# Kernel optimization log

Hardware: AMD Instinct MI355X
Metric: run time of the kernel (lower is better)

## Reference

```python
import jax, jax.numpy as jnp
import numpy as np

DIM = 128
H = 8
NEG_SLOPE = 0.2
SCALE = 12.0
N_ITEMS = 81920
E_INT = 163840
N_T = 4096
NUM_NODE = 40000


def _normalize(x, eps=1e-12):
    n = jnp.linalg.norm(x, axis=-1, keepdims=True)
    return x / jnp.maximum(n, eps)


def _gat(feat, src, dst, fc_w, attn_l, attn_r, bias):
    # GATConv with residual (Identity, since in_feats == out_feats) and bias.
    N = feat.shape[0]
    fs = (feat @ fc_w.T).reshape(N, H, DIM)                # [N,H,D]
    el = jnp.einsum('nhd,hd->nh', fs, attn_l)              # [N,H]
    er = jnp.einsum('nhd,hd->nh', fs, attn_r)              # [N,H]
    e = el[src] + er[dst]                                  # u_add_v -> [E,H]
    e = jnp.where(e >= 0, e, NEG_SLOPE * e)                # leaky_relu
    # edge_softmax grouped by destination node
    emax = jax.ops.segment_max(e, dst, num_segments=N)
    ex = jnp.exp(e - emax[dst])
    denom = jax.ops.segment_sum(ex, dst, num_segments=N)
    a = ex / denom[dst]                                    # [E,H]
    # u_mul_e + sum aggregation
    m = fs[src] * a[:, :, None]                            # [E,H,D]
    rst = jax.ops.segment_sum(m, dst, num_segments=N)      # [N,H,D]
    rst = rst + feat[:, None, :] + bias.reshape(1, H, DIM)
    return rst


def setup_inputs() -> dict:
    key = jax.random.key(0)
    ks = jax.random.split(key, 20)
    stdv = 1.0 / np.sqrt(DIM)

    def unif(k, shape):
        return jax.random.uniform(k, shape, jnp.float32, -stdv, stdv)

    return {
        'iid': jax.random.randint(ks[0], (N_ITEMS,), 0, NUM_NODE),
        'tid': jax.random.randint(ks[1], (N_T,), 0, 10),
        'pid': jax.random.randint(ks[2], (N_ITEMS,), 0, 200),
        'src_i': jax.random.randint(ks[3], (E_INT,), 0, N_ITEMS),
        'dst_i': jax.random.randint(ks[4], (E_INT,), 0, N_ITEMS),
        'agg_src': jnp.arange(N_ITEMS),
        'agg_dst': jnp.sort(jax.random.randint(ks[5], (N_ITEMS,), 0, N_T)),
        'last_nodes': jax.random.randint(ks[6], (N_T,), 0, N_ITEMS),
        'emb': unif(ks[7], (NUM_NODE, DIM)),
        'pos_emb': unif(ks[8], (200, DIM)),
        'target_emb': unif(ks[9], (10, DIM)),
        'gat1_fc': unif(ks[10], (H * DIM, DIM)),
        'gat1_al': unif(ks[11], (H, DIM)),
        'gat1_ar': unif(ks[12], (H, DIM)),
        'gat1_b': jnp.zeros((H * DIM,), jnp.float32),
        'gat2_fc': unif(ks[13], (H * DIM, DIM)),
        'gat2_al': unif(ks[14], (H, DIM)),
        'gat2_ar': unif(ks[15], (H, DIM)),
        'gat2_b': jnp.zeros((H * DIM,), jnp.float32),
        'q_w': unif(ks[16], (DIM, 2 * DIM)),
        'fc_sr_w': unif(ks[17], (DIM, 2 * DIM)),
    }


def reference(iid, tid, pid, src_i, dst_i, agg_src, agg_dst, last_nodes,
              emb, pos_emb, target_emb,
              gat1_fc, gat1_al, gat1_ar, gat1_b,
              gat2_fc, gat2_al, gat2_ar, gat2_b,
              q_w, fc_sr_w):
    h_v = _normalize(emb[iid])                              # [N_items, D]
    h_p = pos_emb[pid]                                      # [E_agg, D]
    h_t = target_emb[tid]                                   # [N_T, D]

    # gat1 on interacts; gat2 on reversed interacts; max over heads each
    h1 = _gat(h_v, src_i, dst_i, gat1_fc, gat1_al, gat1_ar, gat1_b).max(axis=1)
    h2 = _gat(h_v, dst_i, src_i, gat2_fc, gat2_al, gat2_ar, gat2_b).max(axis=1)
    h = _normalize(h1 + h2)                                 # [N_items, D]

    # PosAggregator over 'agg' edges (item -> target)
    ft = h[agg_src]                                         # [E_agg, D]
    e = jnp.tanh(jnp.concatenate([ft, h_p], axis=-1) @ q_w.T)
    w = jnp.sum(e * h_t[agg_dst], axis=-1, keepdims=True)   # udf_agg weight
    sr_g = jax.ops.segment_sum(ft * w, agg_dst, num_segments=h_t.shape[0])
    sr_l = h[last_nodes]                                    # last-item features

    sr = jnp.concatenate([sr_g, sr_l], axis=-1) @ fc_sr_w.T
    scores = SCALE * (_normalize(sr) @ _normalize(emb).T)   # [N_T, num_node]
    return scores
```

## Files before the change

kernel.cpp:

```cpp
#include <hip/hip_runtime.h>
#include <stdint.h>

#define DD 128
#define HN 8
#define NITEMS 81920
#define EINT 163840
#define NT 4096
#define NV 40000
#define NVPAD 40064
#define EAGG 81920
#define NEG_SLOPE 0.2f
#define SCALE 12.0f

typedef unsigned short u16;
typedef __attribute__((ext_vector_type(8))) short bf16x8;
typedef __attribute__((ext_vector_type(4))) float f32x4;
typedef __attribute__((ext_vector_type(4))) unsigned short u16x4;

__device__ __forceinline__ float bf2f(unsigned short u){ return __uint_as_float(((unsigned)u)<<16); }
__device__ __forceinline__ unsigned short f2bf(float f){
  unsigned u = __float_as_uint(f);
  u += 0x7fffu + ((u>>16)&1u);
  return (unsigned short)(u>>16);
}

__global__ __launch_bounds__(256) void k_cast3(const float* __restrict__ fc1, const float* __restrict__ fc2,
    const float* __restrict__ qw, const float* __restrict__ fcsr,
    u16* __restrict__ w1, u16* __restrict__ w2, u16* __restrict__ qb, float* __restrict__ fT){
  int i = blockIdx.x*256 + threadIdx.x;
  if (i < 131072) w1[i] = f2bf(fc1[i]);
  else if (i < 262144) w2[i-131072] = f2bf(fc2[i-131072]);
  else if (i < 294912) qb[i-262144] = f2bf(qw[i-262144]);
  else if (i < 327680){
    int j = i - 294912;
    int k = j >> 7, col = j & 127;
    fT[j] = fcsr[(size_t)col*256 + k];
  }
}

__global__ __launch_bounds__(128) void k_prep_u(const float* __restrict__ fc1, const float* __restrict__ al1,
    const float* __restrict__ ar1, const float* __restrict__ fc2, const float* __restrict__ al2,
    const float* __restrict__ ar2, u16* __restrict__ U){
  int r = blockIdx.x, k = threadIdx.x;
  if (r >= 32){ U[(size_t)r*DD + k] = 0; return; }
  int g = r>>3, h = r&7;
  const float* fc = (g>=2)? fc2 : fc1;
  const float* av = (g==0)? al1 : (g==1)? ar1 : (g==2)? al2 : ar2;
  float s = 0.f;
  for (int d=0; d<DD; ++d) s += fc[(size_t)(h*DD+d)*DD + k] * av[h*DD+d];
  U[(size_t)r*DD + k] = f2bf(s);
}

__global__ __launch_bounds__(256) void k_norm(const float* __restrict__ emb, const int* __restrict__ iid,
    u16* __restrict__ nemb, u16* __restrict__ hvb, int* __restrict__ cnt){
  int gi = blockIdx.x*256 + threadIdx.x;
  if (gi < 2*NITEMS) cnt[gi] = 0;
  int w = gi >> 6;
  int lane = gi & 63;
  u16* dst; const float* src;
  if (w < NVPAD){
    dst = nemb + (size_t)w*DD;
    if (w >= NV){ dst[lane*2]=0; dst[lane*2+1]=0; return; }
    src = emb + (size_t)w*DD;
  } else {
    int n = w - NVPAD;
    dst = hvb + (size_t)n*DD;
    src = emb + (size_t)iid[n]*DD;
  }
  float2 v = *(const float2*)(src + lane*2);
  float ss = v.x*v.x + v.y*v.y;
  #pragma unroll
  for (int m=1;m<64;m<<=1) ss += __shfl_xor(ss, m);
  float inv = 1.f / fmaxf(sqrtf(ss), 1e-12f);
  dst[lane*2]   = f2bf(v.x*inv);
  dst[lane*2+1] = f2bf(v.y*inv);
}

template<int OUT_BF16>
__global__ __launch_bounds__(256) void gemm_nt(const u16* __restrict__ A, const u16* __restrict__ B,
                                               void* __restrict__ C, int M, int N, int K,
                                               float alpha, int ldc, int nvalid){
  __shared__ u16 As[128*32];
  __shared__ u16 Bs[128*32];
  int m0 = blockIdx.x*128, n0 = blockIdx.y*128;
  int t = threadIdx.x, lane = t&63, wid = t>>6;
  int wm = wid>>1, wn = wid&1;
  f32x4 zero = {0.f,0.f,0.f,0.f};
  f32x4 acc[4][4];
  #pragma unroll
  for (int i=0;i<4;i++)
    #pragma unroll
    for (int j=0;j<4;j++) acc[i][j] = zero;
  int lr = lane & 15, lk = (lane>>4)*8;
  for (int k0=0; k0<K; k0+=32){
    #pragma unroll
    for (int cc=0; cc<2; ++cc){
      int c = t + cc*256;
      int row = c>>2, col = (c&3)*8;
      *(bf16x8*)(void*)&As[c*8] = *(const bf16x8*)(const void*)&A[(size_t)(m0+row)*K + k0 + col];
      *(bf16x8*)(void*)&Bs[c*8] = *(const bf16x8*)(const void*)&B[(size_t)(n0+row)*K + k0 + col];
    }
    __syncthreads();
    bf16x8 af[4], bfr[4];
    #pragma unroll
    for (int m=0;m<4;m++) af[m]  = *(const bf16x8*)(const void*)&As[(wm*64+m*16+lr)*32 + lk];
    #pragma unroll
    for (int n=0;n<4;n++) bfr[n] = *(const bf16x8*)(const void*)&Bs[(wn*64+n*16+lr)*32 + lk];
    #pragma unroll
    for (int m=0;m<4;m++)
      #pragma unroll
      for (int n=0;n<4;n++)
        acc[m][n] = __builtin_amdgcn_mfma_f32_16x16x32_bf16(af[m], bfr[n], acc[m][n], 0,0,0);
    __syncthreads();
  }
  #pragma unroll
  for (int m=0;m<4;m++)
    #pragma unroll
    for (int n=0;n<4;n++)
      #pragma unroll
      for (int r=0;r<4;r++){
        int row = m0 + wm*64 + m*16 + (lane>>4)*4 + r;
        int col = n0 + wn*64 + n*16 + (lane&15);
        if (col < nvalid){
          float v = acc[m][n][r]*alpha;
          if (OUT_BF16) ((u16*)C)[(size_t)row*ldc + col] = f2bf(v);
          else          ((float*)C)[(size_t)row*ldc + col] = v;
        }
      }
}

__global__ __launch_bounds__(256) void k_deg2(const int* __restrict__ di, const int* __restrict__ si,
                                              int* __restrict__ cnt){
  int i = blockIdx.x*256+threadIdx.x;
  if (i<EINT){ atomicAdd(&cnt[di[i]],1); atomicAdd(&cnt[NITEMS+si[i]],1); }
}

__global__ __launch_bounds__(256) void k_scan_a(int* cnt, int* off, int* bsum, int n){
  __shared__ int buf[256];
  int b = blockIdx.x, t = threadIdx.x, i = b*256+t;
  int v = (i<n)? cnt[i] : 0;
  buf[t] = v; __syncthreads();
  #pragma unroll
  for (int ofs=1; ofs<256; ofs<<=1){
    int x = (t>=ofs)? buf[t-ofs] : 0;
    __syncthreads();
    buf[t] += x;
    __syncthreads();
  }
  if (i<n){ off[i] = buf[t]-v; cnt[i] = 0; }
  if (t==255) bsum[b] = buf[255];
}

__global__ __launch_bounds__(1024) void k_scan_b(int* bsum, int* off, int nb, int n){
  __shared__ int buf[1024];
  int t = threadIdx.x;
  int v = (t<nb)? bsum[t] : 0;
  buf[t]=v; __syncthreads();
  #pragma unroll
  for (int ofs=1; ofs<1024; ofs<<=1){
    int x=(t>=ofs)?buf[t-ofs]:0; __syncthreads(); buf[t]+=x; __syncthreads();
  }
  if (t<nb) bsum[t] = buf[t]-v;
  if (t==1023) off[n] = buf[1023];
}

__global__ __launch_bounds__(256) void k_scan_c(int* __restrict__ off, const int* __restrict__ bsum, int n){
  int i = blockIdx.x*256+threadIdx.x;
  if (i<n) off[i] += bsum[blockIdx.x];
}

__global__ __launch_bounds__(256) void k_scatter2(const int* __restrict__ di, const int* __restrict__ si,
    const int* __restrict__ off, int* __restrict__ cnt, int* __restrict__ sid){
  int i = blockIdx.x*256+threadIdx.x;
  if (i<EINT){
    int a = di[i];         sid[off[a]+atomicAdd(&cnt[a],1)] = si[i];
    int b = NITEMS+si[i];  sid[off[b]+atomicAdd(&cnt[b],1)] = di[i];
  }
}

__global__ __launch_bounds__(256) void k_aw(const int* __restrict__ off, const int* __restrict__ sid,
    const float* __restrict__ ecat, u16* __restrict__ aw){
  int u = blockIdx.x*256 + threadIdx.x;
  if (u >= 2*NITEMS) return;
  int g = (u >= NITEMS) ? 1 : 0;
  int w = u - g*NITEMS;
  int cl = g*16, cr = g*16 + 8;
  float ern[8];
  #pragma unroll
  for (int h=0;h<8;h++) ern[h] = ecat[(size_t)w*32 + cr + h];
  int lo = off[u], hi = off[u+1];
  float den[8];
  #pragma unroll
  for (int h=0;h<8;h++) den[h] = 0.f;
  for (int i=lo;i<hi;++i){
    const float* e = ecat + (size_t)sid[i]*32 + cl;
    #pragma unroll
    for (int h=0;h<8;h++){
      float lv = e[h] + ern[h];
      lv = (lv>=0.f)? lv : NEG_SLOPE*lv;
      den[h] += expf(lv);
    }
  }
  float inv[8];
  #pragma unroll
  for (int h=0;h<8;h++) inv[h] = (den[h]>0.f)? 1.f/den[h] : 0.f;
  for (int i=lo;i<hi;++i){
    const float* e = ecat + (size_t)sid[i]*32 + cl;
    bf16x8 o;
    #pragma unroll
    for (int h=0;h<8;h++){
      float lv = e[h] + ern[h];
      lv = (lv>=0.f)? lv : NEG_SLOPE*lv;
      o[h] = (short)f2bf(expf(lv)*inv[h]);
    }
    *(bf16x8*)(void*)&aw[(size_t)i*8] = o;
  }
}

__global__ __launch_bounds__(256) void k_agg(const int* __restrict__ off, const int* __restrict__ sid,
    const u16* __restrict__ aw, const u16* __restrict__ hvb, u16* __restrict__ agg, int obase){
  int w = (blockIdx.x*256 + threadIdx.x) >> 6;
  int lane = threadIdx.x & 63;
  if (w >= NITEMS) return;
  int lo = off[obase+w], hi = off[obase+w+1];
  float a0[8], a1[8];
  #pragma unroll
  for (int h=0;h<8;h++){ a0[h]=0.f; a1[h]=0.f; }
  for (int i=lo; i<hi; ++i){
    int s = sid[i];
    unsigned v = *(const unsigned*)(const void*)&hvb[(size_t)s*DD + lane*2];
    float f0 = bf2f((u16)(v & 0xffffu)), f1 = bf2f((u16)(v >> 16));
    bf16x8 w8 = *(const bf16x8*)(const void*)&aw[(size_t)i*8];
    #pragma unroll
    for (int h=0;h<8;h++){
      float wa = bf2f((u16)w8[h]);
      a0[h] += wa*f0; a1[h] += wa*f1;
    }
  }
  #pragma unroll
  for (int h=0;h<8;h++){
    unsigned o = (unsigned)f2bf(a0[h]) | ((unsigned)f2bf(a1[h])<<16);
    *(unsigned*)(void*)&agg[(size_t)w*1024 + h*DD + lane*2] = o;
  }
}

template<int MODE>
__global__ __launch_bounds__(512) void k_hg(const u16* __restrict__ agg, const u16* __restrict__ wfc,
    const float* __restrict__ bias, const u16* __restrict__ hvb,
    u16* __restrict__ h1b, u16* __restrict__ hb){
  __shared__ __align__(16) char smem[52224];
  u16* As = (u16*)smem;
  u16* Bs = As + 64*136;
  float* F = (float*)smem;
  int n0 = blockIdx.x*64;
  int t = threadIdx.x, lane = t&63, wid = t>>6;
  int wm = wid&3, wn = wid>>2;
  int lr = lane&15, lq = lane>>4;
  int ar = t>>3, ak = (t&7)*16;
  f32x4 rm[4];
  #pragma unroll
  for (int n=0;n<4;n++){ f32x4 z={-1e30f,-1e30f,-1e30f,-1e30f}; rm[n]=z; }
  for (int h=0; h<HN; ++h){
    *(bf16x8*)(void*)&As[ar*136 + ak]     = *(const bf16x8*)(const void*)&agg[(size_t)(n0+ar)*1024 + h*DD + ak];
    *(bf16x8*)(void*)&As[ar*136 + ak + 8] = *(const bf16x8*)(const void*)&agg[(size_t)(n0+ar)*1024 + h*DD + ak + 8];
    #pragma unroll
    for (int cc=0; cc<2; ++cc){
      int c = t + cc*512;
      int br = c>>3, bk = (c&7)*16;
      *(bf16x8*)(void*)&Bs[br*136 + bk]     = *(const bf16x8*)(const void*)&wfc[(size_t)(h*DD+br)*DD + bk];
      *(bf16x8*)(void*)&Bs[br*136 + bk + 8] = *(const bf16x8*)(const void*)&wfc[(size_t)(h*DD+br)*DD + bk + 8];
    }
    __syncthreads();
    f32x4 acc[4];
    #pragma unroll
    for (int n=0;n<4;n++){ f32x4 z={0.f,0.f,0.f,0.f}; acc[n]=z; }
    #pragma unroll
    for (int ks=0; ks<4; ++ks){
      bf16x8 af = *(const bf16x8*)(const void*)&As[(wm*16+lr)*136 + ks*32 + lq*8];
      #pragma unroll
      for (int n=0;n<4;n++){
        bf16x8 bfr = *(const bf16x8*)(const void*)&Bs[(wn*64+n*16+lr)*136 + ks*32 + lq*8];
        acc[n] = __builtin_amdgcn_mfma_f32_16x16x32_bf16(af, bfr, acc[n], 0,0,0);
      }
    }
    #pragma unroll
    for (int n=0;n<4;n++){
      float bn = bias[h*DD + wn*64 + n*16 + lr];
      #pragma unroll
      for (int r=0;r<4;r++) rm[n][r] = fmaxf(rm[n][r], acc[n][r] + bn);
    }
    __syncthreads();
  }
  if (MODE==0){
    #pragma unroll
    for (int n=0;n<4;n++)
      #pragma unroll
      for (int r=0;r<4;r++){
        int row = n0 + wm*16 + lq*4 + r;
        int col = wn*64 + n*16 + lr;
        h1b[(size_t)row*DD + col] = f2bf(rm[n][r] + bf2f(hvb[(size_t)row*DD + col]));
      }
  } else {
    #pragma unroll
    for (int n=0;n<4;n++)
      #pragma unroll
      for (int r=0;r<4;r++){
        int lrow = wm*16 + lq*4 + r;
        int col = wn*64 + n*16 + lr;
        int row = n0 + lrow;
        F[lrow*DD + col] = rm[n][r] + bf2f(hvb[(size_t)row*DD + col]) + bf2f(h1b[(size_t)row*DD + col]);
      }
    __syncthreads();
    int r8 = t>>3, q = t&7;
    float vals[16];
    float ss = 0.f;
    #pragma unroll
    for (int j=0;j<16;j++){ vals[j] = F[r8*DD + q*16 + j]; ss += vals[j]*vals[j]; }
    ss += __shfl_xor(ss,1); ss += __shfl_xor(ss,2); ss += __shfl_xor(ss,4);
    float inv = 1.f/fmaxf(sqrtf(ss),1e-12f);
    bf16x8 o0, o1;
    #pragma unroll
    for (int j=0;j<8;j++){ o0[j] = (short)f2bf(vals[j]*inv); o1[j] = (short)f2bf(vals[8+j]*inv); }
    *(bf16x8*)(void*)&hb[(size_t)(n0+r8)*DD + q*16]     = o0;
    *(bf16x8*)(void*)&hb[(size_t)(n0+r8)*DD + q*16 + 8] = o1;
  }
}

__global__ __launch_bounds__(256) void k_epw(const int* __restrict__ asrc, const int* __restrict__ pid,
    const int* __restrict__ adst, const int* __restrict__ tid_, const u16* __restrict__ hb,
    const float* __restrict__ pemb, const u16* __restrict__ qwb, const float* __restrict__ temb,
    float* __restrict__ wv){
  __shared__ u16 As[128*32];
  __shared__ u16 Bs[128*32];
  __shared__ float tembS[10*DD];
  __shared__ float wsum[128];
  __shared__ int rowtt[128];
  int m0 = blockIdx.x*128;
  int t = threadIdx.x, lane = t&63, wid = t>>6;
  int wm = wid>>1, wn = wid&1, lr = lane&15, lq = lane>>4;
  for (int i=t; i<10*DD; i+=256) tembS[i] = temb[i];
  if (t < 128){ rowtt[t] = tid_[adst[m0+t]]; wsum[t] = 0.f; }
  f32x4 zero = {0.f,0.f,0.f,0.f};
  f32x4 acc[4][4];
  #pragma unroll
  for (int i=0;i<4;i++)
    #pragma unroll
    for (int j=0;j<4;j++) acc[i][j] = zero;
  for (int k0=0; k0<256; k0+=32){
    #pragma unroll
    for (int cc=0; cc<2; ++cc){
      int c = t + cc*256;
      int row = c>>2;
      int kk = k0 + (c&3)*8;
      bf16x8 av;
      if (k0 < 128){
        av = *(const bf16x8*)(const void*)&hb[(size_t)asrc[m0+row]*DD + kk];
      } else {
        const float* p = pemb + (size_t)pid[m0+row]*DD + (kk-128);
        float4 p0 = *(const float4*)p;
        float4 p1 = *(const float4*)(p+4);
        av[0]=(short)f2bf(p0.x); av[1]=(short)f2bf(p0.y); av[2]=(short)f2bf(p0.z); av[3]=(short)f2bf(p0.w);
        av[4]=(short)f2bf(p1.x); av[5]=(short)f2bf(p1.y); av[6]=(short)f2bf(p1.z); av[7]=(short)f2bf(p1.w);
      }
      *(bf16x8*)(void*)&As[c*8] = av;
      *(bf16x8*)(void*)&Bs[c*8] = *(const bf16x8*)(const void*)&qwb[(size_t)row*256 + kk];
    }
    __syncthreads();
    bf16x8 af[4], bfr[4];
    #pragma unroll
    for (int m=0;m<4;m++) af[m]  = *(const bf16x8*)(const void*)&As[(wm*64+m*16+lr)*32 + lq*8];
    #pragma unroll
    for (int n=0;n<4;n++) bfr[n] = *(const bf16x8*)(const void*)&Bs[(wn*64+n*16+lr)*32 + lq*8];
    #pragma unroll
    for (int m=0;m<4;m++)
      #pragma unroll
      for (int n=0;n<4;n++)
        acc[m][n] = __builtin_amdgcn_mfma_f32_16x16x32_bf16(af[m], bfr[n], acc[m][n], 0,0,0);
    __syncthreads();
  }
  #pragma unroll
  for (int m=0;m<4;m++)
    #pragma unroll
    for (int r=0;r<4;r++){
      int lrow = wm*64 + m*16 + lq*4 + r;
      int tt = rowtt[lrow];
      float p = 0.f;
      #pragma unroll
      for (int n=0;n<4;n++){
        int col = wn*64 + n*16 + lr;
        p += tanhf(acc[m][n][r]) * tembS[tt*DD + col];
      }
      #pragma unroll
      for (int msk=1; msk<16; msk<<=1) p += __shfl_xor(p, msk);
      if (lr==0) atomicAdd(&wsum[lrow], p);
    }
  __syncthreads();
  if (t < 128) wv[m0+t] = wsum[t];
}

__device__ __forceinline__ int lbound(const int* a, int n, int key){
  int lo=0, hi=n;
  while (lo<hi){ int mid=(lo+hi)>>1; if (a[mid]<key) lo=mid+1; else hi=mid; }
  return lo;
}

__global__ __launch_bounds__(256) void k_sr(const u16* __restrict__ hb, const float* __restrict__ w,
    const int* __restrict__ asrc, const int* __restrict__ adst, const int* __restrict__ lastn,
    const float* __restrict__ fcsrT, u16* __restrict__ nsr){
  __shared__ float cat[256];
  __shared__ float red[128];
  __shared__ int lohi[2];
  int t = blockIdx.x, tid = threadIdx.x;
  if (tid == 0){ lohi[0] = lbound(adst, EAGG, t); lohi[1] = lbound(adst, EAGG, t+1); }
  __syncthreads();
  int lo = lohi[0], hi = lohi[1];
  if (tid < DD){
    float a = 0.f;
    for (int i=lo;i<hi;++i) a += bf2f(hb[(size_t)asrc[i]*DD + tid]) * w[i];
    cat[tid] = a;
  } else {
    int d = tid - DD;
    cat[DD + d] = bf2f(hb[(size_t)lastn[t]*DD + d]);
  }
  __syncthreads();
  float s = 0.f;
  if (tid < DD){
    #pragma unroll 8
    for (int k=0;k<256;++k) s += cat[k]*fcsrT[(size_t)k*DD + tid];
    red[tid] = s*s;
  }
  __syncthreads();
  for (int st=64; st>0; st>>=1){
    if (tid < st) red[tid] += red[tid+st];
    __syncthreads();
  }
  if (tid < DD){
    float inv = 1.f/fmaxf(sqrtf(red[0]),1e-12f);
    nsr[(size_t)t*DD + tid] = f2bf(s*inv);
  }
}

__global__ __launch_bounds__(256) void gemm_sc(const u16* __restrict__ A, const u16* __restrict__ B,
                                               float* __restrict__ C){
  __shared__ __align__(16) char smem[16384];
  u16* As = (u16*)smem;
  u16* Bs = As + 4096;
  float* tr = (float*)smem;
  int flat = blockIdx.y*gridDim.x + blockIdx.x;
  int nf = (flat&7)*1252 + (flat>>3);
  int m0 = (nf & 31)*128;
  int n0 = (nf >> 5)*128;
  int t = threadIdx.x, lane = t&63, wid = t>>6;
  int wm = wid>>1, wn = wid&1, lr = lane&15, lq = lane>>4;
  f32x4 zero = {0.f,0.f,0.f,0.f};
  f32x4 acc[4][4];
  #pragma unroll
  for (int i=0;i<4;i++)
    #pragma unroll
    for (int j=0;j<4;j++) acc[i][j] = zero;
  for (int k0=0; k0<DD; k0+=32){
    #pragma unroll
    for (int cc=0; cc<2; ++cc){
      int c = t + cc*256;
      int row = c>>2, col = (c&3)*8;
      *(bf16x8*)(void*)&As[c*8] = *(const bf16x8*)(const void*)&A[(size_t)(m0+row)*DD + k0 + col];
      *(bf16x8*)(void*)&Bs[c*8] = *(const bf16x8*)(const void*)&B[(size_t)(n0+row)*DD + k0 + col];
    }
    __syncthreads();
    bf16x8 af[4], bfr[4];
    #pragma unroll
    for (int m=0;m<4;m++) af[m]  = *(const bf16x8*)(const void*)&As[(wm*64+m*16+lr)*32 + lq*8];
    #pragma unroll
    for (int n=0;n<4;n++) bfr[n] = *(const bf16x8*)(const void*)&Bs[(wn*64+n*16+lr)*32 + lq*8];
    #pragma unroll
    for (int m=0;m<4;m++)
      #pragma unroll
      for (int n=0;n<4;n++)
        acc[m][n] = __builtin_amdgcn_mfma_f32_16x16x32_bf16(af[m], bfr[n], acc[m][n], 0,0,0);
    __syncthreads();
  }
  #pragma unroll
  for (int m=0;m<4;m++){
    #pragma unroll
    for (int n=0;n<4;n++)
      #pragma unroll
      for (int r=0;r<4;r++)
        tr[wid*1024 + (lq*4+r)*64 + n*16 + lr] = acc[m][n][r]*SCALE;
    __syncthreads();
    int row16 = lane>>2, ch = (lane&3)*16;
    int grow = m0 + wm*64 + m*16 + row16;
    int gcol = n0 + wn*64 + ch;
    if (gcol < NV){
      const float* s = &tr[wid*1024 + row16*64 + ch];
      float* d = &C[(size_t)grow*NV + gcol];
      *(float4*)(d)    = *(const float4*)(s);
      *(float4*)(d+4)  = *(const float4*)(s+4);
      *(float4*)(d+8)  = *(const float4*)(s+8);
      *(float4*)(d+12) = *(const float4*)(s+12);
    }
    __syncthreads();
  }
}

extern "C" void kernel_launch(void* const* d_in, const int* in_sizes, int n_in,
                              void* d_out, int out_size, void* d_ws, size_t ws_size,
                              hipStream_t stream){
  (void)in_sizes; (void)n_in; (void)out_size; (void)ws_size;
  const int*   iid   = (const int*)d_in[0];
  const int*   tid_  = (const int*)d_in[1];
  const int*   pid   = (const int*)d_in[2];
  const int*   src_i = (const int*)d_in[3];
  const int*   dst_i = (const int*)d_in[4];
  const int*   asrc  = (const int*)d_in[5];
  const int*   adst  = (const int*)d_in[6];
  const int*   lastn = (const int*)d_in[7];
  const float* emb   = (const float*)d_in[8];
  const float* pemb  = (const float*)d_in[9];
  const float* temb  = (const float*)d_in[10];
  const float* fc1   = (const float*)d_in[11];
  const float* al1   = (const float*)d_in[12];
  const float* ar1   = (const float*)d_in[13];
  const float* b1    = (const float*)d_in[14];
  const float* fc2   = (const float*)d_in[15];
  const float* al2   = (const float*)d_in[16];
  const float* ar2   = (const float*)d_in[17];
  const float* b2    = (const float*)d_in[18];
  const float* qw    = (const float*)d_in[19];
  const float* fcsr  = (const float*)d_in[20];

  char* ws = (char*)d_ws;
  size_t o = 0;
  auto alc = [&](size_t b)->char*{ char* r = ws + o; o += (b + 511) & ~(size_t)511; return r; };
  u16*   hvb  = (u16*)  alc((size_t)NITEMS*DD*2);
  u16*   hb   = (u16*)  alc((size_t)NITEMS*DD*2);
  u16*   h1b  = (u16*)  alc((size_t)NITEMS*DD*2);
  float* ecat = (float*)alc((size_t)NITEMS*32*4);
  int*   off  = (int*)  alc((size_t)(2*NITEMS+1)*4);
  int*   cnt  = (int*)  alc((size_t)(2*NITEMS)*4);
  int*   bsum = (int*)  alc((size_t)1024*4);
  int*   sid  = (int*)  alc((size_t)(2*EINT)*4);
  u16*   aw   = (u16*)  alc((size_t)(2*EINT)*8*2);
  u16*   wfc1 = (u16*)  alc((size_t)1024*DD*2);
  u16*   wfc2 = (u16*)  alc((size_t)1024*DD*2);
  u16*   qwb  = (u16*)  alc((size_t)DD*256*2);
  float* fT   = (float*)alc((size_t)256*DD*4);
  u16*   Umat = (u16*)  alc((size_t)128*DD*2);
  float* wv   = (float*)alc((size_t)EAGG*4);
  u16*   nsr  = (u16*)  alc((size_t)NT*DD*2);
  u16*   nemb = (u16*)  alc((size_t)NVPAD*DD*2);
  u16*   agg  = (u16*)  alc((size_t)NITEMS*1024*2);

  const int N2 = 2*NITEMS;
  const int NB2 = N2/256;

  k_norm<<<(NVPAD+NITEMS)/4, 256, 0, stream>>>(emb, iid, nemb, hvb, cnt);
  k_prep_u<<<128, 128, 0, stream>>>(fc1, al1, ar1, fc2, al2, ar2, Umat);
  k_cast3<<<1280, 256, 0, stream>>>(fc1, fc2, qw, fcsr, wfc1, wfc2, qwb, fT);
  gemm_nt<0><<<dim3(NITEMS/128, 1), 256, 0, stream>>>(hvb, Umat, ecat, NITEMS, 128, DD, 1.f, 32, 32);

  k_deg2<<<(EINT+255)/256, 256, 0, stream>>>(dst_i, src_i, cnt);
  k_scan_a<<<NB2, 256, 0, stream>>>(cnt, off, bsum, N2);
  k_scan_b<<<1, 1024, 0, stream>>>(bsum, off, NB2, N2);
  k_scan_c<<<NB2, 256, 0, stream>>>(off, bsum, N2);
  k_scatter2<<<(EINT+255)/256, 256, 0, stream>>>(dst_i, src_i, off, cnt, sid);

  k_aw<<<N2/256, 256, 0, stream>>>(off, sid, ecat, aw);

  k_agg<<<NITEMS/4, 256, 0, stream>>>(off, sid, aw, hvb, agg, 0);
  k_hg<0><<<NITEMS/64, 512, 0, stream>>>(agg, wfc1, b1, hvb, h1b, nullptr);
  k_agg<<<NITEMS/4, 256, 0, stream>>>(off, sid, aw, hvb, agg, NITEMS);
  k_hg<1><<<NITEMS/64, 512, 0, stream>>>(agg, wfc2, b2, hvb, h1b, hb);

  k_epw<<<EAGG/128, 256, 0, stream>>>(asrc, pid, adst, tid_, hb, pemb, qwb, temb, wv);
  k_sr<<<NT, 256, 0, stream>>>(hb, wv, asrc, adst, lastn, fT, nsr);

  gemm_sc<<<dim3(32, NVPAD/128), 256, 0, stream>>>(nsr, nemb, (float*)d_out);
}
```

Before: 604.8 us.

## Fuse attention-weight softmax into aggregation kernel and pad gemm_sc transpose buffer

Removes the separate k_aw kernel and its bf16 per-edge attention-weight buffer. Each 64-lane wave now computes the softmax denominators and recomputes exp weights inline while aggregating neighbour features, trading a global write and read for redundant exp work on every lane. The per-wave weights also stay in fp32 instead of being rounded to bf16. Separately, the gemm_sc epilogue staging tile gets a row stride of 65 floats to reduce LDS bank conflicts.

```diff
diff --git a/kernel.cpp b/kernel.cpp
--- a/kernel.cpp
+++ b/kernel.cpp
@@ -178,21 +178,20 @@
   }
 }
 
-__global__ __launch_bounds__(256) void k_aw(const int* __restrict__ off, const int* __restrict__ sid,
-    const float* __restrict__ ecat, u16* __restrict__ aw){
-  int u = blockIdx.x*256 + threadIdx.x;
-  if (u >= 2*NITEMS) return;
-  int g = (u >= NITEMS) ? 1 : 0;
-  int w = u - g*NITEMS;
-  int cl = g*16, cr = g*16 + 8;
+__global__ __launch_bounds__(256) void k_aggw(const int* __restrict__ off, const int* __restrict__ sid,
+    const float* __restrict__ ecat, const u16* __restrict__ hvb, u16* __restrict__ agg,
+    int obase, int cl, int cr){
+  int w = (blockIdx.x*256 + threadIdx.x) >> 6;
+  int lane = threadIdx.x & 63;
+  if (w >= NITEMS) return;
+  int lo = off[obase+w], hi = off[obase+w+1];
   float ern[8];
   #pragma unroll
   for (int h=0;h<8;h++) ern[h] = ecat[(size_t)w*32 + cr + h];
-  int lo = off[u], hi = off[u+1];
   float den[8];
   #pragma unroll
   for (int h=0;h<8;h++) den[h] = 0.f;
-  for (int i=lo;i<hi;++i){
+  for (int i=lo; i<hi; ++i){
     const float* e = ecat + (size_t)sid[i]*32 + cl;
     #pragma unroll
     for (int h=0;h<8;h++){
@@ -204,25 +203,6 @@
   float inv[8];
   #pragma unroll
   for (int h=0;h<8;h++) inv[h] = (den[h]>0.f)? 1.f/den[h] : 0.f;
-  for (int i=lo;i<hi;++i){
-    const float* e = ecat + (size_t)sid[i]*32 + cl;
-    bf16x8 o;
-    #pragma unroll
-    for (int h=0;h<8;h++){
-      float lv = e[h] + ern[h];
-      lv = (lv>=0.f)? lv : NEG_SLOPE*lv;
-      o[h] = (short)f2bf(expf(lv)*inv[h]);
-    }
-    *(bf16x8*)(void*)&aw[(size_t)i*8] = o;
-  }
-}
-
-__global__ __launch_bounds__(256) void k_agg(const int* __restrict__ off, const int* __restrict__ sid,
-    const u16* __restrict__ aw, const u16* __restrict__ hvb, u16* __restrict__ agg, int obase){
-  int w = (blockIdx.x*256 + threadIdx.x) >> 6;
-  int lane = threadIdx.x & 63;
-  if (w >= NITEMS) return;
-  int lo = off[obase+w], hi = off[obase+w+1];
   float a0[8], a1[8];
   #pragma unroll
   for (int h=0;h<8;h++){ a0[h]=0.f; a1[h]=0.f; }
@@ -230,10 +210,12 @@
     int s = sid[i];
     unsigned v = *(const unsigned*)(const void*)&hvb[(size_t)s*DD + lane*2];
     float f0 = bf2f((u16)(v & 0xffffu)), f1 = bf2f((u16)(v >> 16));
-    bf16x8 w8 = *(const bf16x8*)(const void*)&aw[(size_t)i*8];
+    const float* e = ecat + (size_t)s*32 + cl;
     #pragma unroll
     for (int h=0;h<8;h++){
-      float wa = bf2f((u16)w8[h]);
+      float lv = e[h] + ern[h];
+      lv = (lv>=0.f)? lv : NEG_SLOPE*lv;
+      float wa = expf(lv)*inv[h];
       a0[h] += wa*f0; a1[h] += wa*f1;
     }
   }
@@ -442,7 +424,7 @@
 
 __global__ __launch_bounds__(256) void gemm_sc(const u16* __restrict__ A, const u16* __restrict__ B,
                                                float* __restrict__ C){
-  __shared__ __align__(16) char smem[16384];
+  __shared__ __align__(16) char smem[16896];
   u16* As = (u16*)smem;
   u16* Bs = As + 4096;
   float* tr = (float*)smem;
@@ -485,13 +467,13 @@
     for (int n=0;n<4;n++)
       #pragma unroll
       for (int r=0;r<4;r++)
-        tr[wid*1024 + (lq*4+r)*64 + n*16 + lr] = acc[m][n][r]*SCALE;
-    __syncthreads();
-    int row16 = lane>>2, ch = (lane&3)*16;
+        tr[wid*1040 + (lq*4+r)*65 + n*16 + lr] = acc[m][n][r]*SCALE;
+    __syncthreads();
+    int row16 = lane>>2, q = lane&3;
     int grow = m0 + wm*64 + m*16 + row16;
-    int gcol = n0 + wn*64 + ch;
+    int gcol = n0 + wn*64 + q*16;
     if (gcol < NV){
-      const float* s = &tr[wid*1024 + row16*64 + ch];
+      const float* s = &tr[wid*1040 + row16*65 + q*16];
       float* d = &C[(size_t)grow*NV + gcol];
       *(float4*)(d)    = *(const float4*)(s);
       *(float4*)(d+4)  = *(const float4*)(s+4);
@@ -539,7 +521,6 @@
   int*   cnt  = (int*)  alc((size_t)(2*NITEMS)*4);
   int*   bsum = (int*)  alc((size_t)1024*4);
   int*   sid  = (int*)  alc((size_t)(2*EINT)*4);
-  u16*   aw   = (u16*)  alc((size_t)(2*EINT)*8*2);
   u16*   wfc1 = (u16*)  alc((size_t)1024*DD*2);
   u16*   wfc2 = (u16*)  alc((size_t)1024*DD*2);
   u16*   qwb  = (u16*)  alc((size_t)DD*256*2);
@@ -564,11 +545,9 @@
   k_scan_c<<<NB2, 256, 0, stream>>>(off, bsum, N2);
   k_scatter2<<<(EINT+255)/256, 256, 0, stream>>>(dst_i, src_i, off, cnt, sid);
 
-  k_aw<<<N2/256, 256, 0, stream>>>(off, sid, ecat, aw);
-
-  k_agg<<<NITEMS/4, 256, 0, stream>>>(off, sid, aw, hvb, agg, 0);
+  k_aggw<<<NITEMS/4, 256, 0, stream>>>(off, sid, ecat, hvb, agg, 0, 0, 8);
   k_hg<0><<<NITEMS/64, 512, 0, stream>>>(agg, wfc1, b1, hvb, h1b, nullptr);
-  k_agg<<<NITEMS/4, 256, 0, stream>>>(off, sid, aw, hvb, agg, NITEMS);
+  k_aggw<<<NITEMS/4, 256, 0, stream>>>(off, sid, ecat, hvb, agg, NITEMS, 16, 24);
   k_hg<1><<<NITEMS/64, 512, 0, stream>>>(agg, wfc2, b2, hvb, h1b, hb);
 
   k_epw<<<EAGG/128, 256, 0, stream>>>(asrc, pid, adst, tid_, hb, pemb, qwb, temb, wv);
```

After: 711.7 us. 17.7% more time.
